# Performance work log

Measured on AMD Instinct MI355X. Metric: run time of the kernel, lower is better.

Reference implementation:

```python
import jax, jax.numpy as jnp
import numpy as np

EMB_DIM = 768
NUM_HEADS = 12
HEAD_DIM = EMB_DIM // NUM_HEADS
B, S = 8, 1024


def setup_inputs() -> dict:
    key = jax.random.key(0)
    ks = jax.random.split(key, 8)
    q = jax.random.normal(ks[0], (B, S, EMB_DIM), dtype=jnp.float32)
    k = jax.random.normal(ks[1], (B, S, EMB_DIM), dtype=jnp.float32)
    v = jax.random.normal(ks[2], (B, S, EMB_DIM), dtype=jnp.float32)
    # Per-head projection weights, torch nn.Linear layout [out_dim, in_dim]
    xav = float(np.sqrt(6.0 / (HEAD_DIM + HEAD_DIM)))
    Wq = jax.random.uniform(ks[3], (NUM_HEADS, HEAD_DIM, HEAD_DIM), jnp.float32, -xav, xav)
    Wk = jax.random.uniform(ks[4], (NUM_HEADS, HEAD_DIM, HEAD_DIM), jnp.float32, -xav, xav)
    Wv = jax.random.uniform(ks[5], (NUM_HEADS, HEAD_DIM, HEAD_DIM), jnp.float32, -xav, xav)
    # Output projection (torch Linear default init scale not critical for correctness baseline)
    bound = float(1.0 / np.sqrt(EMB_DIM))
    Wo = jax.random.uniform(ks[6], (EMB_DIM, EMB_DIM), jnp.float32, -bound, bound)
    bo = jax.random.uniform(ks[7], (EMB_DIM,), jnp.float32, -bound, bound)
    return {"q": q, "k": k, "v": v, "Wq": Wq, "Wk": Wk, "Wv": Wv, "Wo": Wo, "bo": bo}


def reference(q, k, v, Wq, Wk, Wv, Wo, bo):
    b, s, _ = q.shape
    # split heads: [B, S, E] -> [B, H, S, d]
    def split(x):
        return x.reshape(b, s, NUM_HEADS, HEAD_DIM).transpose(0, 2, 1, 3)
    qh, kh, vh = split(q), split(k), split(v)
    # per-head linear (torch: y = x @ W^T), vectorized over heads
    Q = jnp.einsum('bhsd,hod->bhso', qh, Wq)
    K = jnp.einsum('bhsd,hod->bhso', kh, Wk)
    V = jnp.einsum('bhsd,hod->bhso', vh, Wv)
    scale = 1.0 / jnp.sqrt(jnp.float32(HEAD_DIM))
    scores = jnp.einsum('bhqd,bhkd->bhqk', Q, K) * scale  # [B,H,S,S]
    weights = jax.nn.softmax(scores, axis=-1)
    attn = jnp.einsum('bhqk,bhkd->bhqd', weights, V)
    # merge heads: [B,H,S,d] -> [B,S,E]
    attn = attn.transpose(0, 2, 1, 3).reshape(b, s, EMB_DIM)
    return attn @ Wo.T + bo
```

## Files before the change

### kernel.cpp

```cpp
#include <hip/hip_runtime.h>
#include <hip/hip_bf16.h>

#define BB 8
#define SS 1024
#define EE 768
#define HH 12
#define DD 64
#define NT (BB*SS)

typedef __attribute__((ext_vector_type(8))) short bf16x8;
typedef __attribute__((ext_vector_type(4))) float f32x4;

__device__ __forceinline__ ushort f2bf(float f) {
  union { float f; unsigned u; } x; x.f = f;
  unsigned r = x.u + 0x7fffu + ((x.u >> 16) & 1u);
  return (ushort)(r >> 16);
}

__device__ __forceinline__ unsigned cvtpk(float a, float b) {
  unsigned r;
  asm("v_cvt_pk_bf16_f32 %0, %1, %2" : "=v"(r) : "v"(a), "v"(b));
  return r;
}

__device__ __forceinline__ void gl2lds(const void* g, void* l) {
  __builtin_amdgcn_global_load_lds(
      (const __attribute__((address_space(1))) unsigned int*)g,
      (__attribute__((address_space(3))) unsigned int*)l, 16, 0, 0);
}

#define MFMA16(A, B, C) __builtin_amdgcn_mfma_f32_16x16x32_bf16((A), (B), (C), 0, 0, 0)

__global__ void cvt_weights(const float* __restrict__ Wq, const float* __restrict__ Wk,
                            const float* __restrict__ Wv, const float* __restrict__ Wo,
                            ushort* __restrict__ Wqb, ushort* __restrict__ Wkb,
                            ushort* __restrict__ Wvb, ushort* __restrict__ Wob) {
  int i = blockIdx.x * blockDim.x + threadIdx.x;
  const int NW = HH*DD*DD;
  if (i < NW) { Wqb[i] = f2bf(Wq[i]); Wkb[i] = f2bf(Wk[i]); Wvb[i] = f2bf(Wv[i]); }
  if (i < EE*EE) Wob[i] = f2bf(Wo[i]);
}

__global__ __launch_bounds__(256) void proj_qkv(
    const float* __restrict__ q, const float* __restrict__ k, const float* __restrict__ v,
    const ushort* __restrict__ Wqb, const ushort* __restrict__ Wkb, const ushort* __restrict__ Wvb,
    ushort* __restrict__ Qb, ushort* __restrict__ Kb, ushort* __restrict__ Vt) {
  int bid = blockIdx.x;
  int m  = bid / (BB*HH*(SS/64));
  int r  = bid % (BB*HH*(SS/64));
  int bh = r / (SS/64);
  int st = r % (SS/64);

  const float*  x = (m==0 ? q : (m==1 ? k : v)) + ((size_t)((bh/HH)*SS + st*64))*EE + (bh%HH)*DD;
  const ushort* W = (m==0 ? Wqb : (m==1 ? Wkb : Wvb)) + (bh%HH)*DD*DD;

  int tid = threadIdx.x;
  int w = tid >> 6, l = tid & 63;
  int lr = l & 15, lg = l >> 4;

  union { bf16x8 v; unsigned u[4]; } a[2];
  const float* xr = x + (size_t)(w*16 + lr)*EE;
#pragma unroll
  for (int ks = 0; ks < 2; ++ks) {
    f32x4 t0 = *(const f32x4*)(xr + ks*32 + lg*8);
    f32x4 t1 = *(const f32x4*)(xr + ks*32 + lg*8 + 4);
    a[ks].u[0] = cvtpk(t0[0], t0[1]); a[ks].u[1] = cvtpk(t0[2], t0[3]);
    a[ks].u[2] = cvtpk(t1[0], t1[1]); a[ks].u[3] = cvtpk(t1[2], t1[3]);
  }

  f32x4 acc[4] = {};
  if (m == 2) {
#pragma unroll
    for (int f = 0; f < 4; ++f) {
      bf16x8 b0 = *(const bf16x8*)(W + (f*16 + lr)*DD + lg*8);
      bf16x8 b1 = *(const bf16x8*)(W + (f*16 + lr)*DD + 32 + lg*8);
      acc[f] = MFMA16(a[0].v, b0, acc[f]);
      acc[f] = MFMA16(a[1].v, b1, acc[f]);
    }
    int posb = st*64 + 32*(w>>1) + 8*lg + 4*(w&1);
#pragma unroll
    for (int f = 0; f < 4; ++f) {
      ushort2 p0, p1;
      *(unsigned*)&p0 = cvtpk(acc[f][0], acc[f][1]);
      *(unsigned*)&p1 = cvtpk(acc[f][2], acc[f][3]);
      ushort4 pk; pk.x = p0.x; pk.y = p0.y; pk.z = p1.x; pk.w = p1.y;
      *(ushort4*)(Vt + ((size_t)bh*DD + f*16 + lr)*SS + posb) = pk;
    }
  } else {
#pragma unroll
    for (int f = 0; f < 4; ++f) {
      bf16x8 b0 = *(const bf16x8*)(W + (f*16 + lr)*DD + lg*8);
      bf16x8 b1 = *(const bf16x8*)(W + (f*16 + lr)*DD + 32 + lg*8);
      acc[f] = MFMA16(b0, a[0].v, acc[f]);
      acc[f] = MFMA16(b1, a[1].v, acc[f]);
    }
    float qscale = (m == 0) ? 0.18033688011112042f : 1.0f;
    ushort* dst = (m == 0 ? Qb : Kb) + ((size_t)bh*SS + st*64 + w*16 + lr)*DD;
#pragma unroll
    for (int f = 0; f < 4; ++f) {
      ushort2 p0, p1;
      *(unsigned*)&p0 = cvtpk(acc[f][0]*qscale, acc[f][1]*qscale);
      *(unsigned*)&p1 = cvtpk(acc[f][2]*qscale, acc[f][3]*qscale);
      ushort4 pk; pk.x = p0.x; pk.y = p0.y; pk.z = p1.x; pk.w = p1.y;
      *(ushort4*)(dst + f*16 + lg*4) = pk;
    }
  }
}

__global__ __launch_bounds__(256) void attn_fwd(
    const ushort* __restrict__ Qb, const ushort* __restrict__ Kb,
    const ushort* __restrict__ Vt, ushort* __restrict__ attn) {
  __shared__ uint4 ldsq[3072];
  char* ldsb = (char*)ldsq;

  int bid = blockIdx.x;
  int bh = bid % (BB*HH);
  int qt = bid / (BB*HH);
  int b = bh / HH, h = bh % HH;
  int tid = threadIdx.x, w = tid >> 6, l = tid & 63;
  int lr = l & 15, lg = l >> 4;

  const ushort* Qp0 = Qb + ((size_t)bh*SS + qt*128 + w*32 + lr)*DD;
  bf16x8 bq[2][2];
  bq[0][0] = *(const bf16x8*)(Qp0 + lg*8);
  bq[0][1] = *(const bf16x8*)(Qp0 + 32 + lg*8);
  bq[1][0] = *(const bf16x8*)(Qp0 + 16*DD + lg*8);
  bq[1][1] = *(const bf16x8*)(Qp0 + 16*DD + 32 + lg*8);

  const ushort* Kbh = Kb + (size_t)bh*SS*DD;
  const ushort* Vbh = Vt + (size_t)bh*DD*SS;

  const short ONE = (short)0x3F80;
  bf16x8 ones = {ONE, ONE, ONE, ONE, ONE, ONE, ONE, ONE};

  f32x4 lsum[2] = {};
  f32x4 o[2][4] = {};

#define STAGE(bufidx, kt) do {                                                   \
    char* LK_ = ldsb + (bufidx)*16384;                                           \
    const ushort* ksrc = Kbh + ((size_t)((kt)*64 + w*16 + lr))*DD + lg*8;        \
    const ushort* vsrc = Vbh + ((size_t)(w*16 + lr))*SS + (kt)*64 + lg*8;        \
    gl2lds(ksrc,      LK_ + tid*16);                                             \
    gl2lds(ksrc + 32, LK_ + 4096 + tid*16);                                      \
    gl2lds(vsrc,      LK_ + 8192 + tid*16);                                      \
    gl2lds(vsrc + 32, LK_ + 12288 + tid*16);                                     \
  } while (0)

  STAGE(0, 0);
  STAGE(1, 1);
  int bi = 0;
  for (int kt = 0; kt < 16; ++kt) {
    const char* LK_ = ldsb + bi*16384;
    const char* LV_ = LK_ + 8192;

    if (kt < 15) { asm volatile("s_waitcnt vmcnt(4)" ::: "memory"); }
    else         { asm volatile("s_waitcnt vmcnt(0)" ::: "memory"); }
    __builtin_amdgcn_s_barrier();
    __builtin_amdgcn_sched_barrier(0);

    int pi = bi + 2; if (pi >= 3) pi -= 3;
    if (kt < 14) STAGE(pi, kt + 2);

    f32x4 st0[4] = {}, st1[4] = {};
    __builtin_amdgcn_s_setprio(1);
#pragma unroll
    for (int f = 0; f < 4; ++f) {
      bf16x8 k0 = *(const bf16x8*)(LK_ + f*1024 + l*16);
      bf16x8 k1 = *(const bf16x8*)(LK_ + 4096 + f*1024 + l*16);
      st0[f] = MFMA16(k0, bq[0][0], st0[f]);
      st0[f] = MFMA16(k1, bq[0][1], st0[f]);
      st1[f] = MFMA16(k0, bq[1][0], st1[f]);
      st1[f] = MFMA16(k1, bq[1][1], st1[f]);
    }
    __builtin_amdgcn_s_setprio(0);

    union { bf16x8 v; unsigned u[4]; } pba[2], pbb[2];
#pragma unroll
    for (int s = 0; s < 2; ++s) {
      f32x4* st = (s == 0) ? st0 : st1;
#pragma unroll
      for (int f = 0; f < 4; ++f) {
#pragma unroll
        for (int j = 0; j < 4; ++j) st[f][j] = __builtin_amdgcn_exp2f(st[f][j]);
      }
      pba[s].u[0] = cvtpk(st[0][0], st[0][1]); pba[s].u[1] = cvtpk(st[0][2], st[0][3]);
      pba[s].u[2] = cvtpk(st[1][0], st[1][1]); pba[s].u[3] = cvtpk(st[1][2], st[1][3]);
      pbb[s].u[0] = cvtpk(st[2][0], st[2][1]); pbb[s].u[1] = cvtpk(st[2][2], st[2][3]);
      pbb[s].u[2] = cvtpk(st[3][0], st[3][1]); pbb[s].u[3] = cvtpk(st[3][2], st[3][3]);
    }

    __builtin_amdgcn_s_setprio(1);
#pragma unroll
    for (int f = 0; f < 4; ++f) {
      bf16x8 va = *(const bf16x8*)(LV_ + f*1024 + l*16);
      bf16x8 vc = *(const bf16x8*)(LV_ + 4096 + f*1024 + l*16);
      o[0][f] = MFMA16(va, pba[0].v, o[0][f]);
      o[0][f] = MFMA16(vc, pbb[0].v, o[0][f]);
      o[1][f] = MFMA16(va, pba[1].v, o[1][f]);
      o[1][f] = MFMA16(vc, pbb[1].v, o[1][f]);
    }
    lsum[0] = MFMA16(ones, pba[0].v, lsum[0]);
    lsum[0] = MFMA16(ones, pbb[0].v, lsum[0]);
    lsum[1] = MFMA16(ones, pba[1].v, lsum[1]);
    lsum[1] = MFMA16(ones, pbb[1].v, lsum[1]);
    __builtin_amdgcn_s_setprio(0);

    bi = (bi == 2) ? 0 : bi + 1;
  }
#undef STAGE

#pragma unroll
  for (int s = 0; s < 2; ++s) {
    float inv = 1.0f / lsum[s][0];
    ushort* orow = attn + ((size_t)(b*SS + qt*128 + w*32 + s*16 + lr))*EE + h*DD;
#pragma unroll
    for (int f = 0; f < 4; ++f) {
      ushort4 pkd;
      pkd.x = f2bf(o[s][f][0] * inv);
      pkd.y = f2bf(o[s][f][1] * inv);
      pkd.z = f2bf(o[s][f][2] * inv);
      pkd.w = f2bf(o[s][f][3] * inv);
      *(ushort4*)(orow + f*16 + lg*4) = pkd;
    }
  }
}

__global__ __launch_bounds__(256) void out_proj(
    const ushort* __restrict__ attn, const ushort* __restrict__ Wob,
    const float* __restrict__ bo, float* __restrict__ out) {
  __shared__ uint4 ldsq[3072];
  char* ldsb = (char*)ldsq;

  int bid = blockIdx.x;
  int mt = bid & 127;
  int nt = bid >> 7;
  int tid = threadIdx.x, w = tid >> 6, l = tid & 63;
  int lr = l & 15, lg = l >> 4;

  int rS = tid >> 3;
  int cSw = (((tid & 7) * 16) ^ ((rS & 7) << 4)) >> 1;

  const ushort* Abase = attn + ((size_t)mt*64)*EE;
  const ushort* Bbase = Wob + ((size_t)nt*128)*EE;

#define OSTAGE(bufidx, kt) do {                                                  \
    char* LA_ = ldsb + (bufidx)*24576;                                           \
    char* LB_ = LA_ + 8192;                                                      \
    const ushort* asrc = Abase + (kt)*64 + cSw;                                  \
    const ushort* bsrc = Bbase + (kt)*64 + cSw;                                  \
    gl2lds(asrc + (size_t)rS*EE,        LA_ + tid*16);                           \
    gl2lds(asrc + (size_t)(rS+32)*EE,   LA_ + 4096 + tid*16);                    \
    gl2lds(bsrc + (size_t)rS*EE,        LB_ + tid*16);                           \
    gl2lds(bsrc + (size_t)(rS+32)*EE,   LB_ + 4096 + tid*16);                    \
    gl2lds(bsrc + (size_t)(rS+64)*EE,   LB_ + 8192 + tid*16);                    \
    gl2lds(bsrc + (size_t)(rS+96)*EE,   LB_ + 12288 + tid*16);                   \
  } while (0)

  f32x4 acc[4][2] = {};

#define OCOMPUTE(bufidx) do {                                                    \
    const char* LA_ = ldsb + (bufidx)*24576;                                     \
    const char* LB_ = LA_ + 8192;                                                \
    bf16x8 af[4][2], bf[2][2];                                                   \
    _Pragma("unroll")                                                            \
    for (int f = 0; f < 4; ++f) {                                                \
      int row = f*16 + lr; int sw = (row & 7) << 4;                              \
      af[f][0] = *(const bf16x8*)(LA_ + row*128 + ((lg*16) ^ sw));               \
      af[f][1] = *(const bf16x8*)(LA_ + row*128 + ((64 + lg*16) ^ sw));          \
    }                                                                            \
    _Pragma("unroll")                                                            \
    for (int g = 0; g < 2; ++g) {                                                \
      int row = w*32 + g*16 + lr; int sw = (row & 7) << 4;                       \
      bf[g][0] = *(const bf16x8*)(LB_ + row*128 + ((lg*16) ^ sw));               \
      bf[g][1] = *(const bf16x8*)(LB_ + row*128 + ((64 + lg*16) ^ sw));          \
    }                                                                            \
    _Pragma("unroll")                                                            \
    for (int f = 0; f < 4; ++f) {                                                \
      _Pragma("unroll")                                                          \
      for (int g = 0; g < 2; ++g) {                                              \
        acc[f][g] = MFMA16(af[f][0], bf[g][0], acc[f][g]);                       \
        acc[f][g] = MFMA16(af[f][1], bf[g][1], acc[f][g]);                       \
      }                                                                          \
    }                                                                            \
  } while (0)

  OSTAGE(0, 0);
  for (int kt = 0; kt < EE/64; ++kt) {
    if (kt < EE/64 - 1) OSTAGE((kt + 1) & 1, kt + 1);
    if (kt < EE/64 - 1) { asm volatile("s_waitcnt vmcnt(6)" ::: "memory"); }
    else                { asm volatile("s_waitcnt vmcnt(0)" ::: "memory"); }
    __builtin_amdgcn_s_barrier();
    __builtin_amdgcn_sched_barrier(0);
    OCOMPUTE(kt & 1);
    __builtin_amdgcn_s_barrier();
    __builtin_amdgcn_sched_barrier(0);
  }
#undef OSTAGE
#undef OCOMPUTE

#pragma unroll
  for (int g = 0; g < 2; ++g) {
    int col = nt*128 + w*32 + g*16 + lr;
    float bias = bo[col];
#pragma unroll
    for (int f = 0; f < 4; ++f) {
#pragma unroll
      for (int j = 0; j < 4; ++j) {
        int row = mt*64 + f*16 + lg*4 + j;
        out[(size_t)row*EE + col] = acc[f][g][j] + bias;
      }
    }
  }
}

extern "C" void kernel_launch(void* const* d_in, const int* in_sizes, int n_in,
                              void* d_out, int out_size, void* d_ws, size_t ws_size,
                              hipStream_t stream) {
  (void)in_sizes; (void)n_in; (void)out_size; (void)ws_size;
  const float* q  = (const float*)d_in[0];
  const float* k  = (const float*)d_in[1];
  const float* v  = (const float*)d_in[2];
  const float* Wq = (const float*)d_in[3];
  const float* Wk = (const float*)d_in[4];
  const float* Wv = (const float*)d_in[5];
  const float* Wo = (const float*)d_in[6];
  const float* bo = (const float*)d_in[7];
  float* out = (float*)d_out;

  char* ws = (char*)d_ws;
  const size_t SZ = (size_t)BB*HH*SS*DD*2;
  ushort* Qb   = (ushort*)(ws);
  ushort* Kb   = (ushort*)(ws + SZ);
  ushort* Vt   = (ushort*)(ws + 2*SZ);
  ushort* attn = (ushort*)(ws + 3*SZ);
  ushort* Wqb  = (ushort*)(ws + 4*SZ);
  ushort* Wkb  = (ushort*)(ws + 4*SZ +   98304);
  ushort* Wvb  = (ushort*)(ws + 4*SZ + 2*98304);
  ushort* Wob  = (ushort*)(ws + 4*SZ + 3*98304);

  cvt_weights<<<(EE*EE + 255)/256, 256, 0, stream>>>(Wq, Wk, Wv, Wo, Wqb, Wkb, Wvb, Wob);
  proj_qkv<<<3*BB*HH*(SS/64), 256, 0, stream>>>(q, k, v, Wqb, Wkb, Wvb, Qb, Kb, Vt);
  attn_fwd<<<BB*HH*(SS/128), 256, 0, stream>>>(Qb, Kb, Vt, attn);
  out_proj<<<(NT/64)*(EE/128), 256, 0, stream>>>(attn, Wob, bo, out);
}
```

Measured before the change: 89.81 us.

## Loop projection over four seq tiles per block and split K/V LDS buffering

The QKV projection kernel now has each block process four 64-row sequence tiles instead of one. The per-head weight fragments are loaded once into registers and the next tile's input is prefetched while the current one is computed. This cuts the grid fourfold and the redundant weight loads, at the cost of less parallelism (1152 blocks). In attention, K stays triple-buffered while V moves to double buffering with its own staging, so LDS use drops from 48KB to 40KB, aiming at more resident blocks per CU, with a matching change to the vmcnt wait.

```diff
diff --git a/kernel.cpp b/kernel.cpp
--- a/kernel.cpp
+++ b/kernel.cpp
@@ -46,63 +46,82 @@
     const ushort* __restrict__ Wqb, const ushort* __restrict__ Wkb, const ushort* __restrict__ Wvb,
     ushort* __restrict__ Qb, ushort* __restrict__ Kb, ushort* __restrict__ Vt) {
   int bid = blockIdx.x;
-  int m  = bid / (BB*HH*(SS/64));
-  int r  = bid % (BB*HH*(SS/64));
-  int bh = r / (SS/64);
-  int st = r % (SS/64);
-
-  const float*  x = (m==0 ? q : (m==1 ? k : v)) + ((size_t)((bh/HH)*SS + st*64))*EE + (bh%HH)*DD;
-  const ushort* W = (m==0 ? Wqb : (m==1 ? Wkb : Wvb)) + (bh%HH)*DD*DD;
+  int m  = bid / (BB*HH*4);
+  int r  = bid % (BB*HH*4);
+  int bh = r % (BB*HH);
+  int tg = r / (BB*HH);
+  int b = bh / HH, h = bh % HH;
 
   int tid = threadIdx.x;
   int w = tid >> 6, l = tid & 63;
   int lr = l & 15, lg = l >> 4;
 
-  union { bf16x8 v; unsigned u[4]; } a[2];
-  const float* xr = x + (size_t)(w*16 + lr)*EE;
-#pragma unroll
-  for (int ks = 0; ks < 2; ++ks) {
-    f32x4 t0 = *(const f32x4*)(xr + ks*32 + lg*8);
-    f32x4 t1 = *(const f32x4*)(xr + ks*32 + lg*8 + 4);
-    a[ks].u[0] = cvtpk(t0[0], t0[1]); a[ks].u[1] = cvtpk(t0[2], t0[3]);
-    a[ks].u[2] = cvtpk(t1[0], t1[1]); a[ks].u[3] = cvtpk(t1[2], t1[3]);
-  }
-
-  f32x4 acc[4] = {};
-  if (m == 2) {
-#pragma unroll
-    for (int f = 0; f < 4; ++f) {
-      bf16x8 b0 = *(const bf16x8*)(W + (f*16 + lr)*DD + lg*8);
-      bf16x8 b1 = *(const bf16x8*)(W + (f*16 + lr)*DD + 32 + lg*8);
-      acc[f] = MFMA16(a[0].v, b0, acc[f]);
-      acc[f] = MFMA16(a[1].v, b1, acc[f]);
-    }
-    int posb = st*64 + 32*(w>>1) + 8*lg + 4*(w&1);
-#pragma unroll
-    for (int f = 0; f < 4; ++f) {
-      ushort2 p0, p1;
-      *(unsigned*)&p0 = cvtpk(acc[f][0], acc[f][1]);
-      *(unsigned*)&p1 = cvtpk(acc[f][2], acc[f][3]);
-      ushort4 pk; pk.x = p0.x; pk.y = p0.y; pk.z = p1.x; pk.w = p1.y;
-      *(ushort4*)(Vt + ((size_t)bh*DD + f*16 + lr)*SS + posb) = pk;
-    }
-  } else {
-#pragma unroll
-    for (int f = 0; f < 4; ++f) {
-      bf16x8 b0 = *(const bf16x8*)(W + (f*16 + lr)*DD + lg*8);
-      bf16x8 b1 = *(const bf16x8*)(W + (f*16 + lr)*DD + 32 + lg*8);
-      acc[f] = MFMA16(b0, a[0].v, acc[f]);
-      acc[f] = MFMA16(b1, a[1].v, acc[f]);
-    }
-    float qscale = (m == 0) ? 0.18033688011112042f : 1.0f;
-    ushort* dst = (m == 0 ? Qb : Kb) + ((size_t)bh*SS + st*64 + w*16 + lr)*DD;
-#pragma unroll
-    for (int f = 0; f < 4; ++f) {
-      ushort2 p0, p1;
-      *(unsigned*)&p0 = cvtpk(acc[f][0]*qscale, acc[f][1]*qscale);
-      *(unsigned*)&p1 = cvtpk(acc[f][2]*qscale, acc[f][3]*qscale);
-      ushort4 pk; pk.x = p0.x; pk.y = p0.y; pk.z = p1.x; pk.w = p1.y;
-      *(ushort4*)(dst + f*16 + lg*4) = pk;
+  const float*  xbase = (m==0 ? q : (m==1 ? k : v))
+                      + ((size_t)(b*SS + tg*256 + w*16 + lr))*EE + h*DD;
+  const ushort* W = (m==0 ? Wqb : (m==1 ? Wkb : Wvb)) + h*DD*DD;
+
+  bf16x8 wb0[4], wb1[4];
+#pragma unroll
+  for (int f = 0; f < 4; ++f) {
+    wb0[f] = *(const bf16x8*)(W + (f*16 + lr)*DD + lg*8);
+    wb1[f] = *(const bf16x8*)(W + (f*16 + lr)*DD + 32 + lg*8);
+  }
+
+  f32x4 nx0 = *(const f32x4*)(xbase + lg*8);
+  f32x4 nx1 = *(const f32x4*)(xbase + lg*8 + 4);
+  f32x4 nx2 = *(const f32x4*)(xbase + 32 + lg*8);
+  f32x4 nx3 = *(const f32x4*)(xbase + 36 + lg*8);
+
+  float qscale = (m == 0) ? 0.18033688011112042f : 1.0f;
+
+#pragma unroll
+  for (int t = 0; t < 4; ++t) {
+    f32x4 c0 = nx0, c1 = nx1, c2 = nx2, c3 = nx3;
+    if (t < 3) {
+      const float* xn = xbase + (size_t)(t + 1)*64*EE;
+      nx0 = *(const f32x4*)(xn + lg*8);
+      nx1 = *(const f32x4*)(xn + lg*8 + 4);
+      nx2 = *(const f32x4*)(xn + 32 + lg*8);
+      nx3 = *(const f32x4*)(xn + 36 + lg*8);
+    }
+    union { bf16x8 v; unsigned u[4]; } a0, a1;
+    a0.u[0] = cvtpk(c0[0], c0[1]); a0.u[1] = cvtpk(c0[2], c0[3]);
+    a0.u[2] = cvtpk(c1[0], c1[1]); a0.u[3] = cvtpk(c1[2], c1[3]);
+    a1.u[0] = cvtpk(c2[0], c2[1]); a1.u[1] = cvtpk(c2[2], c2[3]);
+    a1.u[2] = cvtpk(c3[0], c3[1]); a1.u[3] = cvtpk(c3[2], c3[3]);
+
+    f32x4 acc[4] = {};
+    int st = tg*4 + t;
+    if (m == 2) {
+#pragma unroll
+      for (int f = 0; f < 4; ++f) {
+        acc[f] = MFMA16(a0.v, wb0[f], acc[f]);
+        acc[f] = MFMA16(a1.v, wb1[f], acc[f]);
+      }
+      int posb = st*64 + 32*(w>>1) + 8*lg + 4*(w&1);
+#pragma unroll
+      for (int f = 0; f < 4; ++f) {
+        ushort2 p0, p1;
+        *(unsigned*)&p0 = cvtpk(acc[f][0], acc[f][1]);
+        *(unsigned*)&p1 = cvtpk(acc[f][2], acc[f][3]);
+        ushort4 pk; pk.x = p0.x; pk.y = p0.y; pk.z = p1.x; pk.w = p1.y;
+        *(ushort4*)(Vt + ((size_t)bh*DD + f*16 + lr)*SS + posb) = pk;
+      }
+    } else {
+#pragma unroll
+      for (int f = 0; f < 4; ++f) {
+        acc[f] = MFMA16(wb0[f], a0.v, acc[f]);
+        acc[f] = MFMA16(wb1[f], a1.v, acc[f]);
+      }
+      ushort* dst = (m == 0 ? Qb : Kb) + ((size_t)bh*SS + st*64 + w*16 + lr)*DD;
+#pragma unroll
+      for (int f = 0; f < 4; ++f) {
+        ushort2 p0, p1;
+        *(unsigned*)&p0 = cvtpk(acc[f][0]*qscale, acc[f][1]*qscale);
+        *(unsigned*)&p1 = cvtpk(acc[f][2]*qscale, acc[f][3]*qscale);
+        ushort4 pk; pk.x = p0.x; pk.y = p0.y; pk.z = p1.x; pk.w = p1.y;
+        *(ushort4*)(dst + f*16 + lg*4) = pk;
+      }
     }
   }
 }
@@ -110,7 +129,7 @@
 __global__ __launch_bounds__(256) void attn_fwd(
     const ushort* __restrict__ Qb, const ushort* __restrict__ Kb,
     const ushort* __restrict__ Vt, ushort* __restrict__ attn) {
-  __shared__ uint4 ldsq[3072];
+  __shared__ uint4 ldsq[2560];
   char* ldsb = (char*)ldsq;
 
   int bid = blockIdx.x;
@@ -136,37 +155,41 @@
   f32x4 lsum[2] = {};
   f32x4 o[2][4] = {};
 
-#define STAGE(bufidx, kt) do {                                                   \
-    char* LK_ = ldsb + (bufidx)*16384;                                           \
+#define STAGE_K(kbuf, kt) do {                                                   \
+    char* KB_ = ldsb + (kbuf)*8192;                                              \
     const ushort* ksrc = Kbh + ((size_t)((kt)*64 + w*16 + lr))*DD + lg*8;        \
+    gl2lds(ksrc,      KB_ + tid*16);                                             \
+    gl2lds(ksrc + 32, KB_ + 4096 + tid*16);                                      \
+  } while (0)
+#define STAGE_V(vbuf, kt) do {                                                   \
+    char* VB_ = ldsb + 24576 + (vbuf)*8192;                                      \
     const ushort* vsrc = Vbh + ((size_t)(w*16 + lr))*SS + (kt)*64 + lg*8;        \
-    gl2lds(ksrc,      LK_ + tid*16);                                             \
-    gl2lds(ksrc + 32, LK_ + 4096 + tid*16);                                      \
-    gl2lds(vsrc,      LK_ + 8192 + tid*16);                                      \
-    gl2lds(vsrc + 32, LK_ + 12288 + tid*16);                                     \
+    gl2lds(vsrc,      VB_ + tid*16);                                             \
+    gl2lds(vsrc + 32, VB_ + 4096 + tid*16);                                      \
   } while (0)
 
-  STAGE(0, 0);
-  STAGE(1, 1);
-  int bi = 0;
+  STAGE_K(0, 0);
+  STAGE_V(0, 0);
+  STAGE_K(1, 1);
+  int kbuf = 0, vbuf = 0;
   for (int kt = 0; kt < 16; ++kt) {
-    const char* LK_ = ldsb + bi*16384;
-    const char* LV_ = LK_ + 8192;
-
-    if (kt < 15) { asm volatile("s_waitcnt vmcnt(4)" ::: "memory"); }
+    const char* KB_ = ldsb + kbuf*8192;
+    const char* VB_ = ldsb + 24576 + vbuf*8192;
+
+    if (kt < 15) { asm volatile("s_waitcnt vmcnt(2)" ::: "memory"); }
     else         { asm volatile("s_waitcnt vmcnt(0)" ::: "memory"); }
     __builtin_amdgcn_s_barrier();
     __builtin_amdgcn_sched_barrier(0);
 
-    int pi = bi + 2; if (pi >= 3) pi -= 3;
-    if (kt < 14) STAGE(pi, kt + 2);
+    if (kt < 15) STAGE_V(vbuf ^ 1, kt + 1);
+    if (kt < 14) { int nk = kbuf + 2; if (nk >= 3) nk -= 3; STAGE_K(nk, kt + 2); }
 
     f32x4 st0[4] = {}, st1[4] = {};
     __builtin_amdgcn_s_setprio(1);
 #pragma unroll
     for (int f = 0; f < 4; ++f) {
-      bf16x8 k0 = *(const bf16x8*)(LK_ + f*1024 + l*16);
-      bf16x8 k1 = *(const bf16x8*)(LK_ + 4096 + f*1024 + l*16);
+      bf16x8 k0 = *(const bf16x8*)(KB_ + f*1024 + l*16);
+      bf16x8 k1 = *(const bf16x8*)(KB_ + 4096 + f*1024 + l*16);
       st0[f] = MFMA16(k0, bq[0][0], st0[f]);
       st0[f] = MFMA16(k1, bq[0][1], st0[f]);
       st1[f] = MFMA16(k0, bq[1][0], st1[f]);
@@ -192,8 +215,8 @@
     __builtin_amdgcn_s_setprio(1);
 #pragma unroll
     for (int f = 0; f < 4; ++f) {
-      bf16x8 va = *(const bf16x8*)(LV_ + f*1024 + l*16);
-      bf16x8 vc = *(const bf16x8*)(LV_ + 4096 + f*1024 + l*16);
+      bf16x8 va = *(const bf16x8*)(VB_ + f*1024 + l*16);
+      bf16x8 vc = *(const bf16x8*)(VB_ + 4096 + f*1024 + l*16);
       o[0][f] = MFMA16(va, pba[0].v, o[0][f]);
       o[0][f] = MFMA16(vc, pbb[0].v, o[0][f]);
       o[1][f] = MFMA16(va, pba[1].v, o[1][f]);
@@ -205,9 +228,11 @@
     lsum[1] = MFMA16(ones, pbb[1].v, lsum[1]);
     __builtin_amdgcn_s_setprio(0);
 
-    bi = (bi == 2) ? 0 : bi + 1;
-  }
-#undef STAGE
+    kbuf = (kbuf == 2) ? 0 : kbuf + 1;
+    vbuf ^= 1;
+  }
+#undef STAGE_K
+#undef STAGE_V
 
 #pragma unroll
   for (int s = 0; s < 2; ++s) {
@@ -339,7 +364,7 @@
   ushort* Wob  = (ushort*)(ws + 4*SZ + 3*98304);
 
   cvt_weights<<<(EE*EE + 255)/256, 256, 0, stream>>>(Wq, Wk, Wv, Wo, Wqb, Wkb, Wvb, Wob);
-  proj_qkv<<<3*BB*HH*(SS/64), 256, 0, stream>>>(q, k, v, Wqb, Wkb, Wvb, Qb, Kb, Vt);
+  proj_qkv<<<3*BB*HH*4, 256, 0, stream>>>(q, k, v, Wqb, Wkb, Wvb, Qb, Kb, Vt);
   attn_fwd<<<BB*HH*(SS/128), 256, 0, stream>>>(Qb, Kb, Vt, attn);
   out_proj<<<(NT/64)*(EE/128), 256, 0, stream>>>(attn, Wob, bo, out);
 }
```

Result: faster. 82.53 us (-8.1%).
